# Kernel optimization log

Hardware: AMD Instinct MI355X
Metric: run time of the kernel (lower is better)

## Reference

```python
import jax, jax.numpy as jnp
import numpy as np

D_MODEL = 1024
NUM_HEAD = 16
D_K = D_MODEL // NUM_HEAD
FFN_D = 4096
EPS = 1e-5


def _layernorm(x, gamma, beta):
    mu = jnp.mean(x, axis=-1, keepdims=True)
    var = jnp.mean(jnp.square(x - mu), axis=-1, keepdims=True)
    return (x - mu) * jax.lax.rsqrt(var + EPS) * gamma + beta


def setup_inputs() -> dict:
    key = jax.random.key(0)
    ks = jax.random.split(key, 16)
    s = 1.0 / np.sqrt(D_MODEL)
    sf = 1.0 / np.sqrt(FFN_D)
    # weights stored as [in, out] (transpose of torch nn.Linear.weight)
    return {
        "x": jax.random.normal(ks[0], (4, 2048, D_MODEL), dtype=jnp.float32),
        "wq": jax.random.uniform(ks[1], (D_MODEL, D_MODEL), jnp.float32, -s, s),
        "bq": jax.random.uniform(ks[2], (D_MODEL,), jnp.float32, -s, s),
        "wk": jax.random.uniform(ks[3], (D_MODEL, D_MODEL), jnp.float32, -s, s),
        "bk": jax.random.uniform(ks[4], (D_MODEL,), jnp.float32, -s, s),
        "wv": jax.random.uniform(ks[5], (D_MODEL, D_MODEL), jnp.float32, -s, s),
        "bv": jax.random.uniform(ks[6], (D_MODEL,), jnp.float32, -s, s),
        "wo": jax.random.uniform(ks[7], (D_MODEL, D_MODEL), jnp.float32, -s, s),
        "bo": jax.random.uniform(ks[8], (D_MODEL,), jnp.float32, -s, s),
        "w1": jax.random.uniform(ks[9], (D_MODEL, FFN_D), jnp.float32, -s, s),
        "b1": jax.random.uniform(ks[10], (FFN_D,), jnp.float32, -s, s),
        "w2": jax.random.uniform(ks[11], (FFN_D, D_MODEL), jnp.float32, -sf, sf),
        "b2": jax.random.uniform(ks[12], (D_MODEL,), jnp.float32, -sf, sf),
        "g1": jnp.ones((D_MODEL,), jnp.float32),
        "be1": jnp.zeros((D_MODEL,), jnp.float32),
        "g2": jnp.ones((D_MODEL,), jnp.float32),
        "be2": jnp.zeros((D_MODEL,), jnp.float32),
    }


def reference(x, wq, bq, wk, bk, wv, bv, wo, bo, w1, b1, w2, b2, g1, be1, g2, be2):
    B, S, _ = x.shape
    resid1 = x
    # project and split heads: [B, H, S, d_k]
    def heads(w, b):
        return (x @ w + b).reshape(B, S, NUM_HEAD, D_K).transpose(0, 2, 1, 3)
    q = heads(wq, bq)
    k = heads(wk, bk)
    v = heads(wv, bv)
    scores = jnp.einsum("bhsd,bhtd->bhst", q, k) / jnp.sqrt(jnp.float32(D_K))
    attn = jax.nn.softmax(scores, axis=-1)
    ctx = jnp.einsum("bhst,bhtd->bhsd", attn, v)
    ctx = ctx.transpose(0, 2, 1, 3).reshape(B, S, D_MODEL)
    attn_out = ctx @ wo + bo
    x1 = _layernorm(resid1 + attn_out, g1, be1)
    ffn = jax.nn.relu(x1 @ w1 + b1) @ w2 + b2
    return _layernorm(x1 + ffn, g2, be2)
```

## Files before the change

kernel.cpp:

```cpp
#include <hip/hip_runtime.h>

typedef unsigned short u16;
typedef __attribute__((ext_vector_type(8))) u16 u16x8;
typedef __attribute__((ext_vector_type(8))) __bf16 bf16x8;
typedef __attribute__((ext_vector_type(4))) float floatx4;
typedef __attribute__((ext_vector_type(16))) float floatx16;
typedef __attribute__((ext_vector_type(4))) unsigned int u32x4;

#define MFMA16(a, b, c) __builtin_amdgcn_mfma_f32_16x16x32_bf16( \
    __builtin_bit_cast(bf16x8, a), __builtin_bit_cast(bf16x8, b), c, 0, 0, 0)
#define MFMA32(a, b, c) __builtin_amdgcn_mfma_f32_32x32x16_bf16( \
    __builtin_bit_cast(bf16x8, a), __builtin_bit_cast(bf16x8, b), c, 0, 0, 0)

#if __has_builtin(__builtin_amdgcn_exp2f)
#define EXP2(x) __builtin_amdgcn_exp2f(x)
#else
#define EXP2(x) exp2f(x)
#endif

__device__ __forceinline__ float bf2f(u16 h) {
  unsigned u = ((unsigned)h) << 16;
  float f;
  __builtin_memcpy(&f, &u, 4);
  return f;
}
__device__ __forceinline__ u16 f2bf(float f) {
  unsigned u;
  __builtin_memcpy(&u, &f, 4);
  u += 0x7fff + ((u >> 16) & 1);
  return (u16)(u >> 16);
}

__device__ __forceinline__ unsigned cvt_pk_bf16(float a, float b) {
  unsigned r;
  asm("v_cvt_pk_bf16_f32 %0, %1, %2" : "=v"(r) : "v"(a), "v"(b));
  return r;
}
__device__ __forceinline__ void pl32_swap(unsigned& a, unsigned& b) {
  asm("v_permlane32_swap_b32 %0, %1" : "+v"(a), "+v"(b));
}

typedef __attribute__((address_space(1))) const unsigned int gas_u32;
typedef __attribute__((address_space(3))) unsigned int las_u32;

__device__ __forceinline__ void gld_lds16(const u16* g, u16* l) {
  __builtin_amdgcn_global_load_lds((gas_u32*)g, (las_u32*)l, 16, 0, 0);
}

__global__ __launch_bounds__(256) void transpose_k(const float* __restrict__ in,
                                                   u16* __restrict__ out, int R, int C) {
  __shared__ u16 tile[64][65];
  int c0 = blockIdx.x * 64, r0 = blockIdx.y * 64;
  int tc = threadIdx.x & 63, tr = threadIdx.x >> 6;
#pragma unroll
  for (int i = 0; i < 16; ++i)
    tile[tr + i * 4][tc] = f2bf(in[(size_t)(r0 + tr + i * 4) * C + c0 + tc]);
  __syncthreads();
#pragma unroll
  for (int i = 0; i < 16; ++i)
    out[(size_t)(c0 + tr + i * 4) * R + r0 + tc] = tile[tc][tr + i * 4];
}

__global__ __launch_bounds__(256) void transpose4_k(const float* __restrict__ i0,
                                                    const float* __restrict__ i1,
                                                    const float* __restrict__ i2,
                                                    const float* __restrict__ i3,
                                                    u16* __restrict__ o0, u16* __restrict__ o1,
                                                    u16* __restrict__ o2, u16* __restrict__ o3) {
  __shared__ u16 tile[64][65];
  const float* in;
  u16* out;
  switch (blockIdx.z) {
    case 0: in = i0; out = o0; break;
    case 1: in = i1; out = o1; break;
    case 2: in = i2; out = o2; break;
    default: in = i3; out = o3; break;
  }
  int c0 = blockIdx.x * 64, r0 = blockIdx.y * 64;
  int tc = threadIdx.x & 63, tr = threadIdx.x >> 6;
#pragma unroll
  for (int i = 0; i < 16; ++i)
    tile[tr + i * 4][tc] = f2bf(in[(size_t)(r0 + tr + i * 4) * 1024 + c0 + tc]);
  __syncthreads();
#pragma unroll
  for (int i = 0; i < 16; ++i)
    out[(size_t)(c0 + tr + i * 4) * 1024 + r0 + tc] = tile[tc][tr + i * 4];
}

__global__ __launch_bounds__(256) void convert_k(const float* __restrict__ in,
                                                 u16* __restrict__ out) {
  size_t idx = ((size_t)blockIdx.x * 256 + threadIdx.x) * 8;
  floatx4 f0 = *(const floatx4*)(in + idx);
  floatx4 f1 = *(const floatx4*)(in + idx + 4);
  u16x8 o;
#pragma unroll
  for (int e = 0; e < 4; ++e) o[e] = f2bf(f0[e]);
#pragma unroll
  for (int e = 0; e < 4; ++e) o[4 + e] = f2bf(f1[e]);
  *(u16x8*)(out + idx) = o;
}

template <bool C_F32, bool BIAS_ROW>
__global__ __launch_bounds__(256, 2) void gemm_bt(const u16* __restrict__ A,
                                                  const u16* __restrict__ BT,
                                                  const float* __restrict__ bias,
                                                  const float* __restrict__ bias2, int bsplit,
                                                  void* __restrict__ Cv, int M, int N, int K,
                                                  int relu) {
  __shared__ __align__(16) u16 As[2][128 * 64];
  __shared__ __align__(16) u16 Bs[2][128 * 64];
  const int tid = threadIdx.x, lane = tid & 63, wave = tid >> 6;
  const int quad = lane >> 4, l15 = lane & 15;
  const int wr = wave >> 1, wc = wave & 1;
  const int m0 = blockIdx.x * 128, n0 = blockIdx.y * 128;

  floatx4 acc[4][4] = {};

  auto stage = [&](int kt, int buf) {
    int k0 = kt * 64;
#pragma unroll
    for (int p = 0; p < 4; ++p) {
      int chunk = p * 256 + tid;
      int row = chunk >> 3, cc = chunk & 7;
      int gc = cc ^ (row & 7);
      int ldsoff = (p * 256 + wave * 64) * 8;
      gld_lds16(A + (size_t)(m0 + row) * K + k0 + gc * 8, &As[buf][ldsoff]);
      gld_lds16(BT + (size_t)(n0 + row) * K + k0 + gc * 8, &Bs[buf][ldsoff]);
    }
  };

  const int nk = K >> 6;
  stage(0, 0);

  for (int kt = 0; kt < nk; ++kt) {
    const int cur = kt & 1;
    __syncthreads();
    if (kt + 1 < nk) stage(kt + 1, cur ^ 1);

#pragma unroll
    for (int ks = 0; ks < 2; ++ks) {
      u16x8 af[4], bfr[4];
#pragma unroll
      for (int i = 0; i < 4; ++i) {
        int r = wr * 64 + i * 16 + l15;
        af[i] = *(const u16x8*)(&As[cur][r * 64 + (((ks * 4 + quad) ^ (r & 7)) * 8)]);
      }
#pragma unroll
      for (int j = 0; j < 4; ++j) {
        int r = wc * 64 + j * 16 + l15;
        bfr[j] = *(const u16x8*)(&Bs[cur][r * 64 + (((ks * 4 + quad) ^ (r & 7)) * 8)]);
      }
#pragma unroll
      for (int i = 0; i < 4; ++i)
#pragma unroll
        for (int j = 0; j < 4; ++j) acc[i][j] = MFMA16(af[i], bfr[j], acc[i][j]);
    }
  }

#pragma unroll
  for (int j = 0; j < 4; ++j) {
    int col = n0 + wc * 64 + j * 16 + l15;
    float bv = 0.f;
    if (!BIAS_ROW) bv = col < bsplit ? bias[col] : bias2[col - bsplit];
#pragma unroll
    for (int i = 0; i < 4; ++i) {
      int row = m0 + wr * 64 + i * 16 + quad * 4;
#pragma unroll
      for (int r = 0; r < 4; ++r) {
        float v = acc[i][j][r] + (BIAS_ROW ? bias[row + r] : bv);
        if (relu) v = fmaxf(v, 0.f);
        if (C_F32)
          ((float*)Cv)[(size_t)(row + r) * N + col] = v;
        else
          ((u16*)Cv)[(size_t)(row + r) * N + col] = f2bf(v);
      }
    }
  }
}

__global__ __launch_bounds__(256, 4) void attn_k(const u16* __restrict__ Q,
                                                 const u16* __restrict__ Km,
                                                 const u16* __restrict__ Vt,
                                                 u16* __restrict__ O) {
  __shared__ __align__(16) u16 sh[16384];
  const int tid = threadIdx.x, lane = tid & 63, w = tid >> 6;
  const int hi = lane >> 5, l31 = lane & 31;
  const int b = blockIdx.z, h = blockIdx.y, q0 = blockIdx.x * 128;
  const size_t tokbase = (size_t)b * 2048;

#pragma unroll
  for (int p = 0; p < 4; ++p) {
    int chunk = p * 256 + tid, row = chunk >> 3, cc = chunk & 7;
    int gc = cc ^ (row & 7);
    gld_lds16(Q + (tokbase + q0 + row) * 2048 + h * 64 + gc * 8, sh + (p * 256 + w * 64) * 8);
  }
  __syncthreads();
  u16x8 qf[4];
#pragma unroll
  for (int kt = 0; kt < 4; ++kt) {
    int r = w * 32 + l31;
    int sel = (kt * 2 + hi) ^ (r & 7);
    u16x8 t = *(const u16x8*)(sh + r * 64 + sel * 8);
#pragma unroll
    for (int e = 0; e < 8; ++e) t[e] = f2bf(bf2f(t[e]) * 0.18033688011f);
    qf[kt] = t;
  }
  __syncthreads();

  floatx16 oacc0 = {}, oacc1 = {};
  float lsum = 0.f;

  auto stage = [&](int it2, int buf) {
    int t0 = it2 * 64;
#pragma unroll
    for (int p = 0; p < 2; ++p) {
      int chunk = p * 256 + tid;
      int row = chunk >> 3, cc = chunk & 7;
      int gc = cc ^ (row & 7);
      int ldsoff = (p * 256 + w * 64) * 8;
      gld_lds16(Km + (tokbase + t0 + row) * 2048 + h * 64 + gc * 8, sh + buf * 4096 + ldsoff);
      gld_lds16(Vt + ((size_t)(h * 64 + row)) * 8192 + tokbase + t0 + gc * 8,
                sh + 8192 + buf * 4096 + ldsoff);
    }
  };

  stage(0, 0);

  for (int it = 0; it < 32; ++it) {
    const int cur = it & 1;
    __syncthreads();
    if (it + 1 < 32) stage(it + 1, cur ^ 1);
    const u16* kb = sh + cur * 4096;
    const u16* vb = sh + 8192 + cur * 4096;

    u32x4 pf[4];
#pragma unroll
    for (int tt = 0; tt < 2; ++tt) {
      u16x8 ka[4];
#pragma unroll
      for (int kt = 0; kt < 4; ++kt) {
        int r = tt * 32 + l31;
        ka[kt] = *(const u16x8*)(kb + r * 64 + (((kt * 2 + hi) ^ (r & 7)) * 8));
      }
      floatx16 s = {};
      __builtin_amdgcn_s_setprio(1);
#pragma unroll
      for (int kt = 0; kt < 4; ++kt) s = MFMA32(ka[kt], qf[kt], s);
      __builtin_amdgcn_s_setprio(0);

      float p[16];
#pragma unroll
      for (int r = 0; r < 16; ++r) p[r] = EXP2(s[r]);
#pragma unroll
      for (int r = 0; r < 16; ++r) lsum += p[r];
#pragma unroll
      for (int half = 0; half < 2; ++half) {
        unsigned X0 = cvt_pk_bf16(p[half * 8 + 0], p[half * 8 + 1]);
        unsigned X1 = cvt_pk_bf16(p[half * 8 + 2], p[half * 8 + 3]);
        unsigned Y0 = cvt_pk_bf16(p[half * 8 + 4], p[half * 8 + 5]);
        unsigned Y1 = cvt_pk_bf16(p[half * 8 + 6], p[half * 8 + 7]);
        pl32_swap(X0, Y0);
        pl32_swap(X1, Y1);
        u32x4 f;
        f[0] = X0; f[1] = X1; f[2] = Y0; f[3] = Y1;
        pf[tt * 2 + half] = f;
      }
    }

    {
      u16x8 va[4];
#pragma unroll
      for (int kt = 0; kt < 4; ++kt) {
        int r = l31;
        va[kt] = *(const u16x8*)(vb + r * 64 + (((kt * 2 + hi) ^ (r & 7)) * 8));
      }
      __builtin_amdgcn_s_setprio(1);
#pragma unroll
      for (int kt = 0; kt < 4; ++kt)
        oacc0 = MFMA32(va[kt], __builtin_bit_cast(u16x8, pf[kt]), oacc0);
      __builtin_amdgcn_s_setprio(0);
#pragma unroll
      for (int kt = 0; kt < 4; ++kt) {
        int r = 32 + l31;
        va[kt] = *(const u16x8*)(vb + r * 64 + (((kt * 2 + hi) ^ (r & 7)) * 8));
      }
      __builtin_amdgcn_s_setprio(1);
#pragma unroll
      for (int kt = 0; kt < 4; ++kt)
        oacc1 = MFMA32(va[kt], __builtin_bit_cast(u16x8, pf[kt]), oacc1);
      __builtin_amdgcn_s_setprio(0);
    }
  }

  __syncthreads();
  float tot = lsum + __shfl_xor(lsum, 32);
  float inv = 1.0f / fmaxf(tot, 1e-30f);
  const int qrow = w * 32 + l31;
#pragma unroll
  for (int dt = 0; dt < 2; ++dt) {
    const floatx16& oa = dt ? oacc1 : oacc0;
#pragma unroll
    for (int pr = 0; pr < 8; ++pr) {
      float a = oa[2 * pr] * inv, bb = oa[2 * pr + 1] * inv;
      unsigned pkw = (unsigned)f2bf(a) | ((unsigned)f2bf(bb) << 16);
      int d = dt * 32 + (pr & 1) * 2 + (pr >> 1) * 8 + 4 * hi;
      *(unsigned*)(sh + qrow * 72 + d) = pkw;
    }
  }
  __syncthreads();
#pragma unroll
  for (int p2 = 0; p2 < 4; ++p2) {
    int c = p2 * 64 + lane, rl = c >> 3, cc = c & 7;
    u16x8 vv = *(const u16x8*)(sh + (w * 32 + rl) * 72 + cc * 8);
    *(u16x8*)(O + (tokbase + q0 + w * 32 + rl) * 1024 + h * 64 + cc * 8) = vv;
  }
}

template <bool A_F32, bool B_F32, bool OUT_F32>
__global__ __launch_bounds__(256) void ln_k(const void* __restrict__ Av,
                                            const void* __restrict__ Bv,
                                            const float* __restrict__ g,
                                            const float* __restrict__ be,
                                            void* __restrict__ outv) {
  const int lane = threadIdx.x & 63, wave = threadIdx.x >> 6;
  const size_t row = (size_t)blockIdx.x * 4 + wave;
  const size_t base = row * 1024 + lane * 16;
  float v[16];
  if (A_F32) {
    const float* a = (const float*)Av + base;
#pragma unroll
    for (int q = 0; q < 4; ++q) {
      floatx4 t = *(const floatx4*)(a + q * 4);
#pragma unroll
      for (int e = 0; e < 4; ++e) v[q * 4 + e] = t[e];
    }
  } else {
    const u16* a = (const u16*)Av + base;
    u16x8 a0 = *(const u16x8*)a, a1 = *(const u16x8*)(a + 8);
#pragma unroll
    for (int e = 0; e < 8; ++e) {
      v[e] = bf2f(a0[e]);
      v[e + 8] = bf2f(a1[e]);
    }
  }
  if (B_F32) {
    const float* bb = (const float*)Bv + base;
#pragma unroll
    for (int q = 0; q < 4; ++q) {
      floatx4 t = *(const floatx4*)(bb + q * 4);
#pragma unroll
      for (int e = 0; e < 4; ++e) v[q * 4 + e] += t[e];
    }
  } else {
    const u16* bb = (const u16*)Bv + base;
    u16x8 b0 = *(const u16x8*)bb, b1 = *(const u16x8*)(bb + 8);
#pragma unroll
    for (int e = 0; e < 8; ++e) {
      v[e] += bf2f(b0[e]);
      v[e + 8] += bf2f(b1[e]);
    }
  }
  float sum = 0.f, sq = 0.f;
#pragma unroll
  for (int e = 0; e < 16; ++e) {
    sum += v[e];
    sq += v[e] * v[e];
  }
#pragma unroll
  for (int mk = 1; mk < 64; mk <<= 1) {
    sum += __shfl_xor(sum, mk);
    sq += __shfl_xor(sq, mk);
  }
  float mu = sum * (1.f / 1024.f);
  float var = fmaxf(sq * (1.f / 1024.f) - mu * mu, 0.f);
  float rstd = rsqrtf(var + 1e-5f);
  if (OUT_F32) {
    float* o = (float*)outv + base;
#pragma unroll
    for (int q = 0; q < 4; ++q) {
      floatx4 t;
#pragma unroll
      for (int e = 0; e < 4; ++e) {
        int c = lane * 16 + q * 4 + e;
        t[e] = (v[q * 4 + e] - mu) * rstd * g[c] + be[c];
      }
      *(floatx4*)(o + q * 4) = t;
    }
  } else {
    u16x8 o0, o1;
#pragma unroll
    for (int e = 0; e < 8; ++e) {
      int c = lane * 16 + e;
      o0[e] = f2bf((v[e] - mu) * rstd * g[c] + be[c]);
      o1[e] = f2bf((v[e + 8] - mu) * rstd * g[c + 8] + be[c + 8]);
    }
    *(u16x8*)((u16*)outv + base) = o0;
    *(u16x8*)((u16*)outv + base + 8) = o1;
  }
}

extern "C" void kernel_launch(void* const* d_in, const int* in_sizes, int n_in, void* d_out,
                              int out_size, void* d_ws, size_t ws_size, hipStream_t stream) {
  const float* x = (const float*)d_in[0];
  const float* wq = (const float*)d_in[1];
  const float* bq = (const float*)d_in[2];
  const float* wk = (const float*)d_in[3];
  const float* bk = (const float*)d_in[4];
  const float* wv = (const float*)d_in[5];
  const float* bv = (const float*)d_in[6];
  const float* wo = (const float*)d_in[7];
  const float* bo = (const float*)d_in[8];
  const float* w1 = (const float*)d_in[9];
  const float* b1 = (const float*)d_in[10];
  const float* w2 = (const float*)d_in[11];
  const float* b2 = (const float*)d_in[12];
  const float* g1 = (const float*)d_in[13];
  const float* be1 = (const float*)d_in[14];
  const float* g2 = (const float*)d_in[15];
  const float* be2 = (const float*)d_in[16];
  float* out = (float*)d_out;

  u16* W = (u16*)d_ws;
  const size_t M1 = (size_t)1 << 20;
  u16* wqT = W;
  u16* wkT = wqT + M1;
  u16* wvT = wkT + M1;
  u16* woT = wvT + M1;
  u16* w1T = woT + M1;
  u16* w2T = w1T + 4 * M1;
  u16* arena = w2T + 4 * M1;
  const size_t S8M = (size_t)8 << 20;
  u16* xb = arena;
  u16* QKb = arena + S8M;
  u16* Vtb = arena + 3 * S8M;
  u16* Cb = arena + 4 * S8M;
  u16* AO = arena + 5 * S8M;
  u16* X1 = xb;
  u16* F1 = QKb;
  const int NOSPLIT = 1 << 30;

  dim3 blk(256);
  transpose4_k<<<dim3(16, 16, 4), blk, 0, stream>>>(wq, wk, wv, wo, wqT, wkT, wvT, woT);
  transpose_k<<<dim3(64, 16), blk, 0, stream>>>(w1, w1T, 1024, 4096);
  transpose_k<<<dim3(16, 64), blk, 0, stream>>>(w2, w2T, 4096, 1024);
  convert_k<<<4096, blk, 0, stream>>>(x, xb);

  gemm_bt<false, false><<<dim3(64, 16), blk, 0, stream>>>(xb, wqT, bq, bk, 1024, QKb, 8192,
                                                          2048, 1024, 0);
  gemm_bt<false, true><<<dim3(8, 64), blk, 0, stream>>>(wvT, xb, bv, bv, NOSPLIT, Vtb, 1024,
                                                        8192, 1024, 0);

  attn_k<<<dim3(16, 16, 4), blk, 0, stream>>>(QKb, QKb + 1024, Vtb, Cb);

  gemm_bt<false, false><<<dim3(64, 8), blk, 0, stream>>>(Cb, woT, bo, bo, NOSPLIT, AO, 8192,
                                                         1024, 1024, 0);
  ln_k<true, false, false><<<2048, blk, 0, stream>>>(x, AO, g1, be1, X1);

  gemm_bt<false, false><<<dim3(64, 32), blk, 0, stream>>>(X1, w1T, b1, b1, NOSPLIT, F1, 8192,
                                                          4096, 1024, 1);
  gemm_bt<true, false><<<dim3(64, 8), blk, 0, stream>>>(F1, w2T, b2, b2, NOSPLIT, out, 8192,
                                                        1024, 4096, 0);
  ln_k<false, true, true><<<2048, blk, 0, stream>>>(X1, out, g2, be2, out);
}
```

Before: 503.2 us.

## Add 256x256-tile ping-pong GEMM kernel for QK and FFN1 projections

Adds a new 512-thread GEMM kernel with 256x256 output tiles and double-buffered LDS fed by direct global-to-LDS loads. Its main loop interleaves MFMA quarter-steps with staged loads, using explicit barriers, waitcnts and setprio. It replaces the 128-tile kernel for the fused Q/K projection and the first FFN GEMM, aiming for more reuse per loaded byte and better overlap of loads with math. The cost is a large LDS footprint (128 KB per block), which limits occupancy, plus a hand-tuned barrier and waitcnt schedule that could stall or be fragile.

Measured after the change: 513.5 us. 2.0% more time.

```diff
diff --git a/kernel.cpp b/kernel.cpp
--- a/kernel.cpp
+++ b/kernel.cpp
@@ -46,6 +46,10 @@
 __device__ __forceinline__ void gld_lds16(const u16* g, u16* l) {
   __builtin_amdgcn_global_load_lds((gas_u32*)g, (las_u32*)l, 16, 0, 0);
 }
+
+#define SBAR asm volatile("s_barrier" ::: "memory")
+#define LGKM0 asm volatile("s_waitcnt lgkmcnt(0)" ::: "memory")
+#define VMC4 asm volatile("s_waitcnt vmcnt(4)" ::: "memory")
 
 __global__ __launch_bounds__(256) void transpose_k(const float* __restrict__ in,
                                                    u16* __restrict__ out, int R, int C) {
@@ -173,6 +177,153 @@
           ((float*)Cv)[(size_t)(row + r) * N + col] = v;
         else
           ((u16*)Cv)[(size_t)(row + r) * N + col] = f2bf(v);
+      }
+    }
+  }
+}
+
+__global__ __launch_bounds__(512, 2) void gemm256_k(const u16* __restrict__ A,
+                                                    const u16* __restrict__ BT,
+                                                    const float* __restrict__ bias,
+                                                    const float* __restrict__ bias2, int bsplit,
+                                                    u16* __restrict__ C, int M, int N, int K,
+                                                    int relu) {
+  __shared__ __align__(16) u16 As[2][256 * 64];
+  __shared__ __align__(16) u16 Bs[2][256 * 64];
+  const int tid = threadIdx.x, lane = tid & 63, wave = tid >> 6;
+  const int quad = lane >> 4, l15 = lane & 15;
+  const int wm = wave >> 2, wn = wave & 3;
+  const int m0 = blockIdx.x * 256, n0 = blockIdx.y * 256;
+
+  floatx4 acc[8][4] = {};
+
+  auto stageA = [&](int kt, int buf, int h) {
+#pragma unroll
+    for (int p = 0; p < 2; ++p) {
+      int idx = p * 512 + tid;
+      int row = h * 128 + (idx >> 3), cc = idx & 7, gc = cc ^ (row & 7);
+      gld_lds16(A + (size_t)(m0 + row) * K + kt * 64 + gc * 8,
+                &As[buf][(h * 1024 + p * 512 + wave * 64) * 8]);
+    }
+  };
+  auto stageB = [&](int kt, int buf, int h) {
+#pragma unroll
+    for (int p = 0; p < 2; ++p) {
+      int idx = p * 512 + tid;
+      int row = h * 128 + (idx >> 3), cc = idx & 7, gc = cc ^ (row & 7);
+      gld_lds16(BT + (size_t)(n0 + row) * K + kt * 64 + gc * 8,
+                &Bs[buf][(h * 1024 + p * 512 + wave * 64) * 8]);
+    }
+  };
+
+  u16x8 af0[8], af1[8], bl[2][2], bh[2][2];
+  auto rdA = [&](u16x8(&af)[8], int buf, int ks) {
+#pragma unroll
+    for (int i = 0; i < 8; ++i) {
+      int r = wm * 128 + i * 16 + l15;
+      af[i] = *(const u16x8*)(&As[buf][r * 64 + (((ks * 4 + quad) ^ (r & 7)) * 8)]);
+    }
+  };
+  auto rdB = [&](u16x8(&bb)[2], int buf, int ks, int jb) {
+#pragma unroll
+    for (int j = 0; j < 2; ++j) {
+      int r = wn * 64 + (jb + j) * 16 + l15;
+      bb[j] = *(const u16x8*)(&Bs[buf][r * 64 + (((ks * 4 + quad) ^ (r & 7)) * 8)]);
+    }
+  };
+  auto mm = [&](u16x8(&af)[8], u16x8(&bb)[2], int jb) {
+    __builtin_amdgcn_s_setprio(1);
+#pragma unroll
+    for (int i = 0; i < 8; ++i)
+#pragma unroll
+      for (int j = 0; j < 2; ++j) acc[i][jb + j] = MFMA16(af[i], bb[j], acc[i][jb + j]);
+    __builtin_amdgcn_s_setprio(0);
+  };
+
+  const int nk = K >> 6;
+  stageA(0, 0, 0);
+  stageA(0, 0, 1);
+  stageB(0, 0, 0);
+  stageB(0, 0, 1);
+  stageA(1, 1, 0);
+  stageA(1, 1, 1);
+  VMC4;
+  SBAR;
+
+  for (int J = 0; J < (nk >> 1); ++J) {
+    const int t1 = 2 * J + 1;
+    const int t2 = 2 * J + 2 < nk ? 2 * J + 2 : nk - 1;
+    const int t3 = 2 * J + 3 < nk ? 2 * J + 3 : nk - 1;
+    rdA(af0, 0, 0);
+    rdB(bl[0], 0, 0, 0);
+    rdB(bl[1], 0, 1, 0);
+    stageB(t1, 1, 0);
+    SBAR;
+    LGKM0;
+    mm(af0, bl[0], 0);
+    SBAR;
+    rdA(af1, 0, 1);
+    stageB(t1, 1, 1);
+    SBAR;
+    LGKM0;
+    mm(af1, bl[1], 0);
+    SBAR;
+    rdB(bh[0], 0, 0, 2);
+    rdB(bh[1], 0, 1, 2);
+    stageA(t2, 0, 0);
+    SBAR;
+    LGKM0;
+    mm(af0, bh[0], 2);
+    SBAR;
+    stageA(t2, 0, 1);
+    SBAR;
+    LGKM0;
+    mm(af1, bh[1], 2);
+    VMC4;
+    SBAR;
+    rdA(af0, 1, 0);
+    rdB(bl[0], 1, 0, 0);
+    rdB(bl[1], 1, 1, 0);
+    stageB(t2, 0, 0);
+    SBAR;
+    LGKM0;
+    mm(af0, bl[0], 0);
+    SBAR;
+    rdA(af1, 1, 1);
+    stageB(t2, 0, 1);
+    SBAR;
+    LGKM0;
+    mm(af1, bl[1], 0);
+    SBAR;
+    rdB(bh[0], 1, 0, 2);
+    rdB(bh[1], 1, 1, 2);
+    stageA(t3, 1, 0);
+    SBAR;
+    LGKM0;
+    mm(af0, bh[0], 2);
+    SBAR;
+    stageA(t3, 1, 1);
+    SBAR;
+    LGKM0;
+    mm(af1, bh[1], 2);
+    VMC4;
+    SBAR;
+  }
+
+  asm volatile("s_waitcnt vmcnt(0)" ::: "memory");
+
+#pragma unroll
+  for (int j = 0; j < 4; ++j) {
+    int col = n0 + wn * 64 + j * 16 + l15;
+    float bv = col < bsplit ? bias[col] : bias2[col - bsplit];
+#pragma unroll
+    for (int i = 0; i < 8; ++i) {
+      int row = m0 + wm * 128 + i * 16 + quad * 4;
+#pragma unroll
+      for (int r = 0; r < 4; ++r) {
+        float v = acc[i][j][r] + bv;
+        if (relu) v = fmaxf(v, 0.f);
+        C[(size_t)(row + r) * N + col] = f2bf(v);
       }
     }
   }
@@ -445,8 +596,8 @@
   transpose_k<<<dim3(16, 64), blk, 0, stream>>>(w2, w2T, 4096, 1024);
   convert_k<<<4096, blk, 0, stream>>>(x, xb);
 
-  gemm_bt<false, false><<<dim3(64, 16), blk, 0, stream>>>(xb, wqT, bq, bk, 1024, QKb, 8192,
-                                                          2048, 1024, 0);
+  gemm256_k<<<dim3(32, 8), dim3(512), 0, stream>>>(xb, wqT, bq, bk, 1024, QKb, 8192, 2048,
+                                                   1024, 0);
   gemm_bt<false, true><<<dim3(8, 64), blk, 0, stream>>>(wvT, xb, bv, bv, NOSPLIT, Vtb, 1024,
                                                         8192, 1024, 0);
 
@@ -456,8 +607,8 @@
                                                          1024, 1024, 0);
   ln_k<true, false, false><<<2048, blk, 0, stream>>>(x, AO, g1, be1, X1);
 
-  gemm_bt<false, false><<<dim3(64, 32), blk, 0, stream>>>(X1, w1T, b1, b1, NOSPLIT, F1, 8192,
-                                                          4096, 1024, 1);
+  gemm256_k<<<dim3(32, 16), dim3(512), 0, stream>>>(X1, w1T, b1, b1, NOSPLIT, F1, 8192, 4096,
+                                                    1024, 1);
   gemm_bt<true, false><<<dim3(64, 8), blk, 0, stream>>>(F1, w2T, b2, b2, NOSPLIT, out, 8192,
                                                         1024, 4096, 0);
   ln_k<false, true, true><<<2048, blk, 0, stream>>>(X1, out, g2, be2, out);
```

## Add 256x256-tile GEMM kernel for QK projection and FFN up-projection

Applied to the files above, without the earlier changes.

Adds a new GEMM kernel using 1024-thread blocks with 256x256 output tiles, double-buffered LDS staging and XOR-swizzled layout. It is used for the Q/K projection and the first FFN GEMM in place of the 128-tile gemm_bt. Larger tiles give more data reuse per global load. The cost is 128 KB of LDS per block, which allows only one block per CU, fewer blocks in the grid (256 and 512), and possible tail or occupancy effects.

Measured after the change: 495.4 us. Within noise of the previous version (-1.5%).

```diff
diff --git a/kernel.cpp b/kernel.cpp
--- a/kernel.cpp
+++ b/kernel.cpp
@@ -173,6 +173,79 @@
           ((float*)Cv)[(size_t)(row + r) * N + col] = v;
         else
           ((u16*)Cv)[(size_t)(row + r) * N + col] = f2bf(v);
+      }
+    }
+  }
+}
+
+__global__ __launch_bounds__(1024, 4) void gemm256_k(const u16* __restrict__ A,
+                                                     const u16* __restrict__ BT,
+                                                     const float* __restrict__ bias,
+                                                     const float* __restrict__ bias2,
+                                                     int bsplit, u16* __restrict__ C, int M,
+                                                     int N, int K, int relu) {
+  __shared__ __align__(16) u16 As[2][256 * 64];
+  __shared__ __align__(16) u16 Bs[2][256 * 64];
+  const int tid = threadIdx.x, lane = tid & 63, wave = tid >> 6;
+  const int quad = lane >> 4, l15 = lane & 15;
+  const int wm = wave >> 2, wn = wave & 3;
+  const int m0 = blockIdx.x * 256, n0 = blockIdx.y * 256;
+
+  floatx4 acc[4][4] = {};
+
+  auto stage = [&](int kt, int buf) {
+    int k0 = kt * 64;
+#pragma unroll
+    for (int p = 0; p < 2; ++p) {
+      int chunk = p * 1024 + tid;
+      int row = chunk >> 3, cc = chunk & 7;
+      int gc = cc ^ (row & 7);
+      int ldsoff = (p * 1024 + wave * 64) * 8;
+      gld_lds16(A + (size_t)(m0 + row) * K + k0 + gc * 8, &As[buf][ldsoff]);
+      gld_lds16(BT + (size_t)(n0 + row) * K + k0 + gc * 8, &Bs[buf][ldsoff]);
+    }
+  };
+
+  const int nk = K >> 6;
+  stage(0, 0);
+
+  for (int kt = 0; kt < nk; ++kt) {
+    const int cur = kt & 1;
+    __syncthreads();
+    if (kt + 1 < nk) stage(kt + 1, cur ^ 1);
+
+#pragma unroll
+    for (int ks = 0; ks < 2; ++ks) {
+      u16x8 af[4], bfr[4];
+#pragma unroll
+      for (int i = 0; i < 4; ++i) {
+        int r = wm * 64 + i * 16 + l15;
+        af[i] = *(const u16x8*)(&As[cur][r * 64 + (((ks * 4 + quad) ^ (r & 7)) * 8)]);
+      }
+#pragma unroll
+      for (int j = 0; j < 4; ++j) {
+        int r = wn * 64 + j * 16 + l15;
+        bfr[j] = *(const u16x8*)(&Bs[cur][r * 64 + (((ks * 4 + quad) ^ (r & 7)) * 8)]);
+      }
+#pragma unroll
+      for (int i = 0; i < 4; ++i)
+#pragma unroll
+        for (int j = 0; j < 4; ++j) acc[i][j] = MFMA16(af[i], bfr[j], acc[i][j]);
+    }
+  }
+
+#pragma unroll
+  for (int j = 0; j < 4; ++j) {
+    int col = n0 + wn * 64 + j * 16 + l15;
+    float bv = col < bsplit ? bias[col] : bias2[col - bsplit];
+#pragma unroll
+    for (int i = 0; i < 4; ++i) {
+      int row = m0 + wm * 64 + i * 16 + quad * 4;
+#pragma unroll
+      for (int r = 0; r < 4; ++r) {
+        float v = acc[i][j][r] + bv;
+        if (relu) v = fmaxf(v, 0.f);
+        C[(size_t)(row + r) * N + col] = f2bf(v);
       }
     }
   }
@@ -445,8 +518,8 @@
   transpose_k<<<dim3(16, 64), blk, 0, stream>>>(w2, w2T, 4096, 1024);
   convert_k<<<4096, blk, 0, stream>>>(x, xb);
 
-  gemm_bt<false, false><<<dim3(64, 16), blk, 0, stream>>>(xb, wqT, bq, bk, 1024, QKb, 8192,
-                                                          2048, 1024, 0);
+  gemm256_k<<<dim3(32, 8), dim3(1024), 0, stream>>>(xb, wqT, bq, bk, 1024, QKb, 8192, 2048,
+                                                    1024, 0);
   gemm_bt<false, true><<<dim3(8, 64), blk, 0, stream>>>(wvT, xb, bv, bv, NOSPLIT, Vtb, 1024,
                                                         8192, 1024, 0);
 
@@ -456,8 +529,8 @@
                                                          1024, 1024, 0);
   ln_k<true, false, false><<<2048, blk, 0, stream>>>(x, AO, g1, be1, X1);
 
-  gemm_bt<false, false><<<dim3(64, 32), blk, 0, stream>>>(X1, w1T, b1, b1, NOSPLIT, F1, 8192,
-                                                          4096, 1024, 1);
+  gemm256_k<<<dim3(32, 16), dim3(1024), 0, stream>>>(X1, w1T, b1, b1, NOSPLIT, F1, 8192, 4096,
+                                                     1024, 1);
   gemm_bt<true, false><<<dim3(64, 8), blk, 0, stream>>>(F1, w2T, b2, b2, NOSPLIT, out, 8192,
                                                         1024, 4096, 0);
   ln_k<false, true, true><<<2048, blk, 0, stream>>>(X1, out, g2, be2, out);
```

## Double query rows per attention block to reuse K/V tiles; merge FFN weight transposes

Applied to the files above, without the earlier changes.

The attention kernel now handles 256 query rows per block (64 per wave, as two 32-row groups), so each K/V tile staged in LDS and each K/V fragment read from LDS feeds twice as many MFMAs. The grid halves and launch bounds drop to 2 blocks per CU to leave room for the doubled accumulators and Q fragments. The cost is higher register pressure and fewer blocks (512) to spread across the CUs. Separately, the two FFN weight transpose launches are merged into one kernel launch.

After: 497.3 us. About the same (-1.2%).

```diff
diff --git a/kernel.cpp b/kernel.cpp
--- a/kernel.cpp
+++ b/kernel.cpp
@@ -45,20 +45,6 @@
 
 __device__ __forceinline__ void gld_lds16(const u16* g, u16* l) {
   __builtin_amdgcn_global_load_lds((gas_u32*)g, (las_u32*)l, 16, 0, 0);
-}
-
-__global__ __launch_bounds__(256) void transpose_k(const float* __restrict__ in,
-                                                   u16* __restrict__ out, int R, int C) {
-  __shared__ u16 tile[64][65];
-  int c0 = blockIdx.x * 64, r0 = blockIdx.y * 64;
-  int tc = threadIdx.x & 63, tr = threadIdx.x >> 6;
-#pragma unroll
-  for (int i = 0; i < 16; ++i)
-    tile[tr + i * 4][tc] = f2bf(in[(size_t)(r0 + tr + i * 4) * C + c0 + tc]);
-  __syncthreads();
-#pragma unroll
-  for (int i = 0; i < 16; ++i)
-    out[(size_t)(c0 + tr + i * 4) * R + r0 + tc] = tile[tc][tr + i * 4];
 }
 
 __global__ __launch_bounds__(256) void transpose4_k(const float* __restrict__ i0,
@@ -87,6 +73,31 @@
     out[(size_t)(c0 + tr + i * 4) * 1024 + r0 + tc] = tile[tc][tr + i * 4];
 }
 
+__global__ __launch_bounds__(256) void transposeW_k(const float* __restrict__ w1,
+                                                    const float* __restrict__ w2,
+                                                    u16* __restrict__ w1T,
+                                                    u16* __restrict__ w2T) {
+  __shared__ u16 tile[64][65];
+  const float* in;
+  u16* out;
+  int R, C, r0, c0;
+  if (blockIdx.z == 0) {
+    in = w1; out = w1T; R = 1024; C = 4096;
+    c0 = blockIdx.x * 64; r0 = blockIdx.y * 64;
+  } else {
+    in = w2; out = w2T; R = 4096; C = 1024;
+    r0 = blockIdx.x * 64; c0 = blockIdx.y * 64;
+  }
+  int tc = threadIdx.x & 63, tr = threadIdx.x >> 6;
+#pragma unroll
+  for (int i = 0; i < 16; ++i)
+    tile[tr + i * 4][tc] = f2bf(in[(size_t)(r0 + tr + i * 4) * C + c0 + tc]);
+  __syncthreads();
+#pragma unroll
+  for (int i = 0; i < 16; ++i)
+    out[(size_t)(c0 + tr + i * 4) * R + r0 + tc] = tile[tc][tr + i * 4];
+}
+
 __global__ __launch_bounds__(256) void convert_k(const float* __restrict__ in,
                                                  u16* __restrict__ out) {
   size_t idx = ((size_t)blockIdx.x * 256 + threadIdx.x) * 8;
@@ -178,37 +189,39 @@
   }
 }
 
-__global__ __launch_bounds__(256, 4) void attn_k(const u16* __restrict__ Q,
+__global__ __launch_bounds__(256, 2) void attn_k(const u16* __restrict__ Q,
                                                  const u16* __restrict__ Km,
                                                  const u16* __restrict__ Vt,
                                                  u16* __restrict__ O) {
   __shared__ __align__(16) u16 sh[16384];
   const int tid = threadIdx.x, lane = tid & 63, w = tid >> 6;
   const int hi = lane >> 5, l31 = lane & 31;
-  const int b = blockIdx.z, h = blockIdx.y, q0 = blockIdx.x * 128;
+  const int b = blockIdx.z, h = blockIdx.y, q0 = blockIdx.x * 256;
   const size_t tokbase = (size_t)b * 2048;
 
 #pragma unroll
-  for (int p = 0; p < 4; ++p) {
+  for (int p = 0; p < 8; ++p) {
     int chunk = p * 256 + tid, row = chunk >> 3, cc = chunk & 7;
     int gc = cc ^ (row & 7);
     gld_lds16(Q + (tokbase + q0 + row) * 2048 + h * 64 + gc * 8, sh + (p * 256 + w * 64) * 8);
   }
   __syncthreads();
-  u16x8 qf[4];
-#pragma unroll
-  for (int kt = 0; kt < 4; ++kt) {
-    int r = w * 32 + l31;
-    int sel = (kt * 2 + hi) ^ (r & 7);
-    u16x8 t = *(const u16x8*)(sh + r * 64 + sel * 8);
-#pragma unroll
-    for (int e = 0; e < 8; ++e) t[e] = f2bf(bf2f(t[e]) * 0.18033688011f);
-    qf[kt] = t;
-  }
+  u16x8 qf[2][4];
+#pragma unroll
+  for (int g = 0; g < 2; ++g)
+#pragma unroll
+    for (int kt = 0; kt < 4; ++kt) {
+      int r = w * 64 + g * 32 + l31;
+      int sel = (kt * 2 + hi) ^ (r & 7);
+      u16x8 t = *(const u16x8*)(sh + r * 64 + sel * 8);
+#pragma unroll
+      for (int e = 0; e < 8; ++e) t[e] = f2bf(bf2f(t[e]) * 0.18033688011f);
+      qf[g][kt] = t;
+    }
   __syncthreads();
 
-  floatx16 oacc0 = {}, oacc1 = {};
-  float lsum = 0.f;
+  floatx16 oacc[2][2] = {};
+  float lsum[2] = {};
 
   auto stage = [&](int it2, int buf) {
     int t0 = it2 * 64;
@@ -233,7 +246,7 @@
     const u16* kb = sh + cur * 4096;
     const u16* vb = sh + 8192 + cur * 4096;
 
-    u32x4 pf[4];
+    u32x4 pf[2][4];
 #pragma unroll
     for (int tt = 0; tt < 2; ++tt) {
       u16x8 ka[4];
@@ -242,77 +255,77 @@
         int r = tt * 32 + l31;
         ka[kt] = *(const u16x8*)(kb + r * 64 + (((kt * 2 + hi) ^ (r & 7)) * 8));
       }
-      floatx16 s = {};
+#pragma unroll
+      for (int g = 0; g < 2; ++g) {
+        floatx16 s = {};
+        __builtin_amdgcn_s_setprio(1);
+#pragma unroll
+        for (int kt = 0; kt < 4; ++kt) s = MFMA32(ka[kt], qf[g][kt], s);
+        __builtin_amdgcn_s_setprio(0);
+
+        float p[16];
+#pragma unroll
+        for (int r = 0; r < 16; ++r) p[r] = EXP2(s[r]);
+        float ls = 0.f;
+#pragma unroll
+        for (int r = 0; r < 16; ++r) ls += p[r];
+        lsum[g] += ls;
+#pragma unroll
+        for (int half = 0; half < 2; ++half) {
+          unsigned X0 = cvt_pk_bf16(p[half * 8 + 0], p[half * 8 + 1]);
+          unsigned X1 = cvt_pk_bf16(p[half * 8 + 2], p[half * 8 + 3]);
+          unsigned Y0 = cvt_pk_bf16(p[half * 8 + 4], p[half * 8 + 5]);
+          unsigned Y1 = cvt_pk_bf16(p[half * 8 + 6], p[half * 8 + 7]);
+          pl32_swap(X0, Y0);
+          pl32_swap(X1, Y1);
+          u32x4 f;
+          f[0] = X0; f[1] = X1; f[2] = Y0; f[3] = Y1;
+          pf[g][tt * 2 + half] = f;
+        }
+      }
+    }
+
+#pragma unroll
+    for (int dt = 0; dt < 2; ++dt) {
+      u16x8 va[4];
+#pragma unroll
+      for (int kt = 0; kt < 4; ++kt) {
+        int r = dt * 32 + l31;
+        va[kt] = *(const u16x8*)(vb + r * 64 + (((kt * 2 + hi) ^ (r & 7)) * 8));
+      }
       __builtin_amdgcn_s_setprio(1);
 #pragma unroll
-      for (int kt = 0; kt < 4; ++kt) s = MFMA32(ka[kt], qf[kt], s);
+      for (int g = 0; g < 2; ++g)
+#pragma unroll
+        for (int kt = 0; kt < 4; ++kt)
+          oacc[g][dt] = MFMA32(va[kt], __builtin_bit_cast(u16x8, pf[g][kt]), oacc[g][dt]);
       __builtin_amdgcn_s_setprio(0);
-
-      float p[16];
-#pragma unroll
-      for (int r = 0; r < 16; ++r) p[r] = EXP2(s[r]);
-#pragma unroll
-      for (int r = 0; r < 16; ++r) lsum += p[r];
-#pragma unroll
-      for (int half = 0; half < 2; ++half) {
-        unsigned X0 = cvt_pk_bf16(p[half * 8 + 0], p[half * 8 + 1]);
-        unsigned X1 = cvt_pk_bf16(p[half * 8 + 2], p[half * 8 + 3]);
-        unsigned Y0 = cvt_pk_bf16(p[half * 8 + 4], p[half * 8 + 5]);
-        unsigned Y1 = cvt_pk_bf16(p[half * 8 + 6], p[half * 8 + 7]);
-        pl32_swap(X0, Y0);
-        pl32_swap(X1, Y1);
-        u32x4 f;
-        f[0] = X0; f[1] = X1; f[2] = Y0; f[3] = Y1;
-        pf[tt * 2 + half] = f;
-      }
-    }
-
-    {
-      u16x8 va[4];
-#pragma unroll
-      for (int kt = 0; kt < 4; ++kt) {
-        int r = l31;
-        va[kt] = *(const u16x8*)(vb + r * 64 + (((kt * 2 + hi) ^ (r & 7)) * 8));
-      }
-      __builtin_amdgcn_s_setprio(1);
-#pragma unroll
-      for (int kt = 0; kt < 4; ++kt)
-        oacc0 = MFMA32(va[kt], __builtin_bit_cast(u16x8, pf[kt]), oacc0);
-      __builtin_amdgcn_s_setprio(0);
-#pragma unroll
-      for (int kt = 0; kt < 4; ++kt) {
-        int r = 32 + l31;
-        va[kt] = *(const u16x8*)(vb + r * 64 + (((kt * 2 + hi) ^ (r & 7)) * 8));
-      }
-      __builtin_amdgcn_s_setprio(1);
-#pragma unroll
-      for (int kt = 0; kt < 4; ++kt)
-        oacc1 = MFMA32(va[kt], __builtin_bit_cast(u16x8, pf[kt]), oacc1);
-      __builtin_amdgcn_s_setprio(0);
-    }
-  }
-
-  __syncthreads();
-  float tot = lsum + __shfl_xor(lsum, 32);
-  float inv = 1.0f / fmaxf(tot, 1e-30f);
-  const int qrow = w * 32 + l31;
-#pragma unroll
-  for (int dt = 0; dt < 2; ++dt) {
-    const floatx16& oa = dt ? oacc1 : oacc0;
-#pragma unroll
-    for (int pr = 0; pr < 8; ++pr) {
-      float a = oa[2 * pr] * inv, bb = oa[2 * pr + 1] * inv;
-      unsigned pkw = (unsigned)f2bf(a) | ((unsigned)f2bf(bb) << 16);
-      int d = dt * 32 + (pr & 1) * 2 + (pr >> 1) * 8 + 4 * hi;
-      *(unsigned*)(sh + qrow * 72 + d) = pkw;
-    }
-  }
-  __syncthreads();
-#pragma unroll
-  for (int p2 = 0; p2 < 4; ++p2) {
-    int c = p2 * 64 + lane, rl = c >> 3, cc = c & 7;
-    u16x8 vv = *(const u16x8*)(sh + (w * 32 + rl) * 72 + cc * 8);
-    *(u16x8*)(O + (tokbase + q0 + w * 32 + rl) * 1024 + h * 64 + cc * 8) = vv;
+    }
+  }
+
+#pragma unroll
+  for (int g = 0; g < 2; ++g) {
+    __syncthreads();
+    float tot = lsum[g] + __shfl_xor(lsum[g], 32);
+    float inv = 1.0f / fmaxf(tot, 1e-30f);
+    const int lrow = w * 32 + l31;
+#pragma unroll
+    for (int dt = 0; dt < 2; ++dt) {
+#pragma unroll
+      for (int pr = 0; pr < 8; ++pr) {
+        float a = oacc[g][dt][2 * pr] * inv, bb = oacc[g][dt][2 * pr + 1] * inv;
+        unsigned pkw = (unsigned)f2bf(a) | ((unsigned)f2bf(bb) << 16);
+        int d = dt * 32 + (pr & 1) * 2 + (pr >> 1) * 8 + 4 * hi;
+        *(unsigned*)(sh + lrow * 72 + d) = pkw;
+      }
+    }
+    __syncthreads();
+#pragma unroll
+    for (int p2 = 0; p2 < 4; ++p2) {
+      int c = p2 * 64 + lane, rl = c >> 3, cc = c & 7;
+      u16x8 vv = *(const u16x8*)(sh + (w * 32 + rl) * 72 + cc * 8);
+      *(u16x8*)(O + (tokbase + q0 + w * 64 + g * 32 + rl) * 1024 + h * 64 + cc * 8) = vv;
+    }
   }
 }
 
@@ -441,8 +454,7 @@
 
   dim3 blk(256);
   transpose4_k<<<dim3(16, 16, 4), blk, 0, stream>>>(wq, wk, wv, wo, wqT, wkT, wvT, woT);
-  transpose_k<<<dim3(64, 16), blk, 0, stream>>>(w1, w1T, 1024, 4096);
-  transpose_k<<<dim3(16, 64), blk, 0, stream>>>(w2, w2T, 4096, 1024);
+  transposeW_k<<<dim3(64, 16, 2), blk, 0, stream>>>(w1, w2, w1T, w2T);
   convert_k<<<4096, blk, 0, stream>>>(x, xb);
 
   gemm_bt<false, false><<<dim3(64, 16), blk, 0, stream>>>(xb, wqT, bq, bk, 1024, QKb, 8192,
@@ -450,7 +462,7 @@
   gemm_bt<false, true><<<dim3(8, 64), blk, 0, stream>>>(wvT, xb, bv, bv, NOSPLIT, Vtb, 1024,
                                                         8192, 1024, 0);
 
-  attn_k<<<dim3(16, 16, 4), blk, 0, stream>>>(QKb, QKb + 1024, Vtb, Cb);
+  attn_k<<<dim3(8, 16, 4), blk, 0, stream>>>(QKb, QKb + 1024, Vtb, Cb);
 
   gemm_bt<false, false><<<dim3(64, 8), blk, 0, stream>>>(Cb, woT, bo, bo, NOSPLIT, AO, 8192,
                                                          1024, 1024, 0);
```
